# Performance work log

Measured on AMD Instinct MI355X. Metric: run time of the kernel, lower is better.

## Reference

```python
import jax, jax.numpy as jnp
import numpy as np

B, N, E, D, H, DK, DV = 1, 25000, 400000, 128, 4, 32, 32


def setup_inputs() -> dict:
    key = jax.random.key(0)
    ks = jax.random.split(key, 12)
    s = 1.0 / np.sqrt(D)
    return {
        "edge_indices": jax.random.randint(ks[0], (B, 2, E), 0, N),
        "edge_features": jax.random.normal(ks[1], (B, E, D), jnp.float32),
        "input_Q": jax.random.normal(ks[2], (B, N, D), jnp.float32),
        "input_K": jax.random.normal(ks[3], (B, N, D), jnp.float32),
        "input_V": jax.random.normal(ks[4], (B, N, D), jnp.float32),
        "W_Q": jax.random.normal(ks[5], (H * DK, D), jnp.float32) * s,
        "W_K": jax.random.normal(ks[6], (H * DK, D), jnp.float32) * s,
        "W_V": jax.random.normal(ks[7], (H * DV, D), jnp.float32) * s,
        "W_E": jax.random.normal(ks[8], (H * DV, D), jnp.float32) * s,
        "W_fc": jax.random.normal(ks[9], (D, H * DV), jnp.float32) * (1.0 / np.sqrt(H * DV)),
        "gamma": jnp.ones((D,), jnp.float32),
        "beta": jnp.zeros((D,), jnp.float32),
    }


def reference(edge_indices, edge_features, input_Q, input_K, input_V,
              W_Q, W_K, W_V, W_E, W_fc, gamma, beta):
    b, n, _ = input_Q.shape
    # projections -> [b, h, n, d]
    Q = (input_Q @ W_Q.T).reshape(b, n, H, DK).transpose(0, 2, 1, 3)
    K = (input_K @ W_K.T).reshape(b, n, H, DK).transpose(0, 2, 1, 3)
    V = (input_V @ W_V.T).reshape(b, n, H, DV).transpose(0, 2, 1, 3)
    Ef = (edge_features @ W_E.T).reshape(b, -1, H, DV).transpose(0, 2, 1, 3)  # [b,h,e,dv]
    src = edge_indices[0, 0]  # [e]
    tgt = edge_indices[0, 1]
    Qe = Q[:, :, src, :]  # [b,h,e,dk]
    Ke = K[:, :, tgt, :]
    Ve = V[:, :, tgt, :]
    scores = (Qe * Ke) / np.sqrt(DK) * Ef
    attn = jnp.exp(jnp.clip(scores.sum(-1, keepdims=True), -5.0, 5.0))  # [b,h,e,1]
    msg = attn * Ve
    out = jnp.zeros_like(Q).at[:, :, src, :].add(msg)  # scatter-add over src nodes
    coeff = jnp.zeros((b, H, n, 1), Q.dtype).at[:, :, src, :].add(attn)
    out = out / (coeff + 1e-8)
    out = out.transpose(0, 2, 1, 3).reshape(b, n, H * DV)
    out = out @ W_fc.T
    x = out + input_Q
    mu = x.mean(-1, keepdims=True)
    var = ((x - mu) ** 2).mean(-1, keepdims=True)
    y = (x - mu) / jnp.sqrt(var + 1e-5) * gamma + beta
    return y, attn
```

## Files before the change

### kernel.cpp

```cpp
#include <hip/hip_runtime.h>
#include <hip/hip_bf16.h>
#include <cstdint>
#include <cstddef>

#define EN 400000
#define NN 25000

typedef __attribute__((ext_vector_type(8))) short bf16x8;
typedef __attribute__((ext_vector_type(4))) short bf16x4;
typedef __attribute__((ext_vector_type(4))) float f32x4;
typedef __attribute__((ext_vector_type(4))) _Float16 f16x4;
typedef __attribute__((ext_vector_type(8))) _Float16 f16x8;

__device__ __forceinline__ short f2bf(float f) {
    unsigned int u = __float_as_uint(f);
    u = (u + 0x7fffu + ((u >> 16) & 1u)) >> 16;
    return (short)u;
}
__device__ __forceinline__ float bf2f(short s) {
    return __uint_as_float(((unsigned int)(unsigned short)s) << 16);
}

__device__ __forceinline__ f16x8 pin8h(f16x8 v) {
    union { f16x8 s; int i[4]; } u; u.s = v;
    const int a = (threadIdx.x & 63) << 2;
#pragma unroll
    for (int k = 0; k < 4; ++k) u.i[k] = __builtin_amdgcn_ds_bpermute(a, u.i[k]);
    return u.s;
}

__global__ __launch_bounds__(256) void convert_hist_kernel(
    const float* __restrict__ w0, const float* __restrict__ w1,
    const float* __restrict__ w2, const float* __restrict__ w3,
    const float* __restrict__ w4, _Float16* __restrict__ wf,
    short* __restrict__ wfc,
    const int* __restrict__ eidx, int* __restrict__ deg)
{
    if (blockIdx.x < 320) {
        int i = blockIdx.x * 256 + threadIdx.x;
        int w = i >> 14, off = i & 16383;
        if (w < 4) {
            const float* src = (w == 0) ? w0 : (w == 1) ? w1 : (w == 2) ? w2 : w3;
            wf[i] = (_Float16)src[off];
        } else {
            wfc[off] = f2bf(w4[off]);
        }
    } else {
        int e = (blockIdx.x - 320) * 256 + threadIdx.x;
        if (e < EN) atomicAdd(&deg[eidx[e]], 1);
    }
}

__global__ __launch_bounds__(1024) void scan_kernel(
    const int* __restrict__ deg, int* __restrict__ base)
{
    __shared__ int part[1024];
    const int t = threadIdx.x;
    const int CH = 25;
    int loc[CH];
    int s = 0;
#pragma unroll
    for (int i = 0; i < CH; ++i) {
        int idx = t * CH + i;
        loc[i] = s;
        s += (idx < NN) ? deg[idx] : 0;
    }
    part[t] = s;
    __syncthreads();
    for (int d = 1; d < 1024; d <<= 1) {
        int v = (t >= d) ? part[t - d] : 0;
        __syncthreads();
        part[t] += v;
        __syncthreads();
    }
    int off = (t > 0) ? part[t - 1] : 0;
#pragma unroll
    for (int i = 0; i < CH; ++i) {
        int idx = t * CH + i;
        if (idx < NN) base[idx] = off + loc[i];
    }
    if (t == 1023) base[NN] = part[1023];
}

__global__ __launch_bounds__(256) void scatter_kernel(
    const int* __restrict__ eidx, const int* __restrict__ base,
    int* __restrict__ cnt, int4* __restrict__ pack, int* __restrict__ tgt_csr)
{
    int e = blockIdx.x * 256 + threadIdx.x;
    if (e < EN) {
        int s = eidx[e];
        int tg = eidx[EN + e];
        int p = base[s] + atomicAdd(&cnt[s], 1);
        pack[e] = make_int4(s, tg, p, 0);
        tgt_csr[p] = tg;
    }
}

__global__ __launch_bounds__(256, 4) void proj_all_kernel(
    const float* __restrict__ inQ, const float* __restrict__ inK,
    const float* __restrict__ inV, const _Float16* __restrict__ WfBase,
    _Float16* __restrict__ Qh, _Float16* __restrict__ Kh, _Float16* __restrict__ Vh)
{
    const int mode = blockIdx.y;
    const int lane = threadIdx.x & 63;
    const int hw = threadIdx.x >> 6;
    const int el = lane & 15;
    const int g  = lane >> 4;
    const int ntiles = (NN + 15) >> 4;

    const float* X = (mode == 0) ? inQ : (mode == 1) ? inK : inV;
    const _Float16* Wf = WfBase + mode * 16384;
    _Float16* P = (mode == 0) ? Qh : (mode == 1) ? Kh : Vh;

    f16x8 wf[2][4];
#pragma unroll
    for (int dtt = 0; dtt < 2; ++dtt)
#pragma unroll
        for (int kc = 0; kc < 4; ++kc) {
            const int r = hw * 32 + ((el >> 2) * 8) + dtt * 4 + (el & 3);
            wf[dtt][kc] = pin8h(*(const f16x8*)(Wf + r * 128 + kc * 32 + g * 8));
        }

    for (int tile = blockIdx.x; tile < ntiles; tile += gridDim.x) {
        const int row = tile * 16 + el;
        const int rc = row < NN ? row : NN - 1;
        const float* xrow = X + (size_t)rc * 128;
        f32x4 acc0 = {}, acc1 = {};
#pragma unroll
        for (int kc = 0; kc < 4; ++kc) {
            const int kb = kc * 32 + g * 8;
            f32x4 x0 = *(const f32x4*)(xrow + kb);
            f32x4 x1 = *(const f32x4*)(xrow + kb + 4);
            f16x8 b;
#pragma unroll
            for (int j = 0; j < 4; ++j) { b[j] = (_Float16)x0[j]; b[4 + j] = (_Float16)x1[j]; }
            acc0 = __builtin_amdgcn_mfma_f32_16x16x32_f16(wf[0][kc], b, acc0, 0, 0, 0);
            acc1 = __builtin_amdgcn_mfma_f32_16x16x32_f16(wf[1][kc], b, acc1, 0, 0, 0);
        }
        if (row < NN) {
            f16x8 o;
#pragma unroll
            for (int j = 0; j < 4; ++j) {
                o[j]     = (_Float16)acc0[j];
                o[4 + j] = (_Float16)acc1[j];
            }
            *(f16x8*)(P + (size_t)row * 128 + hw * 32 + g * 8) = o;
        }
    }
}

__global__ __launch_bounds__(512, 2) void edge_score_kernel(
    const int4* __restrict__ pack, const float* __restrict__ efeat,
    const _Float16* __restrict__ Qh, const _Float16* __restrict__ Kh,
    const _Float16* __restrict__ WEf,
    float* __restrict__ attn_out, float* __restrict__ attn_csr)
{
    __shared__ _Float16 lds_e[2][32][136];

    const int t    = threadIdx.x;
    const int lane = t & 63;
    const int w    = t >> 6;
    const int hw   = w & 3;
    const int sub  = w >> 2;
    const int el   = lane & 15;
    const int g    = lane >> 4;
    const int se   = t >> 4;
    const int sd   = (t & 15) * 8;
    const int NT   = EN / 32;

    f16x8 wf[2][4];
#pragma unroll
    for (int dtt = 0; dtt < 2; ++dtt)
#pragma unroll
        for (int kc = 0; kc < 4; ++kc) {
            const int r = hw * 32 + ((el >> 2) * 8) + dtt * 4 + (el & 3);
            wf[dtt][kc] = pin8h(*(const f16x8*)(WEf + r * 128 + kc * 32 + g * 8));
        }

    const int dbase = hw * 32 + g * 8;
    int tile = blockIdx.x;
    int4 pk = pack[(size_t)tile * 32 + sub * 16 + el];

    {
        const float* p = efeat + ((size_t)tile * 32 + se) * 128 + sd;
        f32x4 a = *(const f32x4*)p;
        f32x4 b = *(const f32x4*)(p + 4);
        f16x8 h8;
#pragma unroll
        for (int j = 0; j < 4; ++j) {
            h8[j] = (_Float16)a[j];
            h8[4 + j] = (_Float16)b[j];
        }
        *(f16x8*)&lds_e[0][se][sd] = h8;
    }
    f32x4 eA, eB;
    int4 pk1;
    {
        const int t1 = tile + (int)gridDim.x;
        const int tl1 = (t1 < NT) ? t1 : tile;
        const float* np = efeat + ((size_t)tl1 * 32 + se) * 128 + sd;
        eA = *(const f32x4*)np;
        eB = *(const f32x4*)(np + 4);
        pk1 = pack[(size_t)tl1 * 32 + sub * 16 + el];
    }

    int buf = 0;
    while (true) {
        f16x8 q16 = *(const f16x8*)(Qh + (size_t)pk.x * 128 + dbase);
        f16x8 k16 = *(const f16x8*)(Kh + (size_t)pk.y * 128 + dbase);

        const int next = tile + (int)gridDim.x;
        const bool has_next = next < NT;
        const int n2 = next + (int)gridDim.x;
        const int tl2 = (n2 < NT) ? n2 : tile;
        const float* np2 = efeat + ((size_t)tl2 * 32 + se) * 128 + sd;
        f32x4 eAn = *(const f32x4*)np2;
        f32x4 eBn = *(const f32x4*)(np2 + 4);
        int4 pk2 = pack[(size_t)tl2 * 32 + sub * 16 + el];

        asm volatile("s_waitcnt lgkmcnt(0)" ::: "memory");
        __builtin_amdgcn_s_barrier();
        __builtin_amdgcn_sched_barrier(0);

        __builtin_amdgcn_s_setprio(1);
        f32x4 acc0 = {}, acc1 = {};
#pragma unroll
        for (int kc = 0; kc < 4; ++kc) {
            const int kb = kc * 32 + g * 8;
            f16x8 be = *(const f16x8*)&lds_e[buf][sub * 16 + el][kb];
            acc0 = __builtin_amdgcn_mfma_f32_16x16x32_f16(wf[0][kc], be, acc0, 0, 0, 0);
            acc1 = __builtin_amdgcn_mfma_f32_16x16x32_f16(wf[1][kc], be, acc1, 0, 0, 0);
        }
        __builtin_amdgcn_s_setprio(0);

        float part = 0.f;
#pragma unroll
        for (int j = 0; j < 4; ++j) {
            part += (float)q16[j]     * (float)k16[j]     * acc0[j];
            part += (float)q16[4 + j] * (float)k16[4 + j] * acc1[j];
        }
        part += __shfl_xor(part, 16, 64);
        part += __shfl_xor(part, 32, 64);
        float sc = part * 0.17677669529663687f;
        sc = fminf(5.0f, fmaxf(-5.0f, sc));
        const float a = __expf(sc);

        const int edge = tile * 32 + sub * 16 + el;
        if (g == 0) {
            attn_out[(size_t)hw * EN + edge] = a;
            attn_csr[(size_t)pk.z * 4 + hw] = a;
        }

        if (!has_next) break;

        {
            f16x8 h8;
#pragma unroll
            for (int j = 0; j < 4; ++j) {
                h8[j] = (_Float16)eA[j];
                h8[4 + j] = (_Float16)eB[j];
            }
            *(f16x8*)&lds_e[buf ^ 1][se][sd] = h8;
        }

        tile = next;
        pk = pk1;  pk1 = pk2;
        eA = eAn;  eB = eBn;
        buf ^= 1;
    }
}

__global__ __launch_bounds__(512) void node_kernel(
    const int* __restrict__ base, const int* __restrict__ tgt_csr,
    const float* __restrict__ attn_csr, const _Float16* __restrict__ Vh,
    const short* __restrict__ Wfcb, const float* __restrict__ inQ,
    const float* __restrict__ gamma, const float* __restrict__ beta,
    float* __restrict__ y)
{
    __shared__ short wlds[128 * 136];
    __shared__ float alds[32 * 132];

    const int t = threadIdx.x;
    {
        const int r = t >> 2, colb = (t & 3) * 32;
#pragma unroll
        for (int c = 0; c < 4; ++c) {
            bf16x8 w = *(const bf16x8*)(Wfcb + r * 128 + colb + c * 8);
            *(bf16x8*)(&wlds[r * 136 + colb + c * 8]) = w;
        }
    }

    const int n_l = t >> 4;
    const int el  = t & 15;
    const int node = blockIdx.x * 32 + n_l;

    int b0 = 0, b1 = 0;
    if (node < NN) { b0 = base[node]; b1 = base[node + 1]; }
    float acc[8] = {};
    float csum = 0.f;
    const int h = el >> 2;

    int p = b0;
    for (; p + 8 <= b1; p += 8) {
        int   tg[8];
        float aa[8];
        f16x8 vv[8];
#pragma unroll
        for (int u = 0; u < 8; ++u) tg[u] = tgt_csr[p + u];
#pragma unroll
        for (int u = 0; u < 8; ++u) aa[u] = attn_csr[(size_t)(p + u) * 4 + h];
#pragma unroll
        for (int u = 0; u < 8; ++u) vv[u] = *(const f16x8*)(Vh + (size_t)tg[u] * 128 + el * 8);
#pragma unroll
        for (int u = 0; u < 8; ++u) {
            csum += aa[u];
#pragma unroll
            for (int j = 0; j < 8; ++j) acc[j] += aa[u] * (float)vv[u][j];
        }
    }
    for (; p < b1; ++p) {
        const int tg = tgt_csr[p];
        const float a = attn_csr[(size_t)p * 4 + h];
        f16x8 v = *(const f16x8*)(Vh + (size_t)tg * 128 + el * 8);
        csum += a;
#pragma unroll
        for (int j = 0; j < 8; ++j) acc[j] += a * (float)v[j];
    }

    const float invc = 1.0f / (csum + 1e-8f);
#pragma unroll
    for (int j = 0; j < 8; ++j) alds[n_l * 132 + el * 8 + j] = acc[j] * invc;
    __syncthreads();

    float fc[8] = {};
#pragma unroll 4
    for (int k0 = 0; k0 < 128; k0 += 8) {
        float a8[8];
#pragma unroll
        for (int j = 0; j < 8; ++j) a8[j] = alds[n_l * 132 + k0 + j];
#pragma unroll
        for (int i = 0; i < 8; ++i) {
            const int d = el + 16 * i;
            bf16x8 w = *(const bf16x8*)(&wlds[d * 136 + k0]);
#pragma unroll
            for (int j = 0; j < 8; ++j) fc[i] += a8[j] * bf2f(w[j]);
        }
    }

    if (node < NN) {
        float x[8];
        float s = 0.f, s2 = 0.f;
#pragma unroll
        for (int i = 0; i < 8; ++i) {
            const int d = el + 16 * i;
            x[i] = fc[i] + inQ[(size_t)node * 128 + d];
            s += x[i]; s2 += x[i] * x[i];
        }
        s  += __shfl_xor(s, 1, 64);  s2 += __shfl_xor(s2, 1, 64);
        s  += __shfl_xor(s, 2, 64);  s2 += __shfl_xor(s2, 2, 64);
        s  += __shfl_xor(s, 4, 64);  s2 += __shfl_xor(s2, 4, 64);
        s  += __shfl_xor(s, 8, 64);  s2 += __shfl_xor(s2, 8, 64);
        const float mu = s * (1.0f / 128.0f);
        const float var = s2 * (1.0f / 128.0f) - mu * mu;
        const float rstd = rsqrtf(var + 1e-5f);
#pragma unroll
        for (int i = 0; i < 8; ++i) {
            const int d = el + 16 * i;
            y[(size_t)node * 128 + d] = (x[i] - mu) * rstd * gamma[d] + beta[d];
        }
    }
}

extern "C" void kernel_launch(void* const* d_in, const int* in_sizes, int n_in,
                              void* d_out, int out_size, void* d_ws, size_t ws_size,
                              hipStream_t stream) {
    const int*   eidx  = (const int*)d_in[0];
    const float* efeat = (const float*)d_in[1];
    const float* inQ   = (const float*)d_in[2];
    const float* inK   = (const float*)d_in[3];
    const float* inV   = (const float*)d_in[4];
    const float* WQ    = (const float*)d_in[5];
    const float* WK    = (const float*)d_in[6];
    const float* WV    = (const float*)d_in[7];
    const float* WE    = (const float*)d_in[8];
    const float* Wfc   = (const float*)d_in[9];
    const float* gamma = (const float*)d_in[10];
    const float* beta  = (const float*)d_in[11];

    float* y = (float*)d_out;
    float* attn_out = y + (size_t)NN * 128;

    char* ws = (char*)d_ws;
    _Float16* Qh   = (_Float16*)ws;
    _Float16* Kh   = (_Float16*)(ws + 6400000);
    _Float16* Vh   = (_Float16*)(ws + 12800000);
    _Float16* Wf   = (_Float16*)(ws + 19200000);
    short* Wfcb    = (short*)(ws + 19331072);
    float* attn_csr= (float*)(ws + 19363840);
    int*   tgt_csr = (int*)  (ws + 25763840);
    int4*  pack    = (int4*) (ws + 27363840);
    int*   deg     = (int*)  (ws + 33763840);
    int*   cnt     = (int*)  (ws + 33864192);
    int*   base    = (int*)  (ws + 33964544);

    hipMemsetAsync(deg, 0, 200704, stream);

    convert_hist_kernel<<<320 + (EN + 255) / 256, 256, 0, stream>>>(
        WQ, WK, WV, WE, Wfc, Wf, Wfcb, eidx, deg);
    scan_kernel<<<1, 1024, 0, stream>>>(deg, base);
    scatter_kernel<<<(EN + 255) / 256, 256, 0, stream>>>(eidx, base, cnt, pack, tgt_csr);

    dim3 pg(391, 3);
    proj_all_kernel<<<pg, 256, 0, stream>>>(inQ, inK, inV, Wf, Qh, Kh, Vh);

    edge_score_kernel<<<768, 512, 0, stream>>>(pack, efeat, Qh, Kh, Wf + 3 * 16384,
                                               attn_out, attn_csr);

    node_kernel<<<(NN + 31) / 32, 512, 0, stream>>>(base, tgt_csr, attn_csr, Vh,
                                                    Wfcb, inQ, gamma, beta, y);
}
```

Baseline: 218.9 us.

## Split prefix scan across blocks and degree-sort nodes for node kernel

Replaces the single-block degree scan with a three-kernel multi-block scan. It also builds a degree histogram and uses it to counting-sort node ids by degree. The node kernel then processes nodes in degree order, so the 16-lane groups in a block have similar edge-loop lengths and less load imbalance. This adds two extra kernel launches and an indirection through nodeord. The sorted order also changes which rows sit near each other in memory accesses.

```diff
diff --git a/kernel.cpp b/kernel.cpp
--- a/kernel.cpp
+++ b/kernel.cpp
@@ -7,9 +7,7 @@
 #define NN 25000
 
 typedef __attribute__((ext_vector_type(8))) short bf16x8;
-typedef __attribute__((ext_vector_type(4))) short bf16x4;
 typedef __attribute__((ext_vector_type(4))) float f32x4;
-typedef __attribute__((ext_vector_type(4))) _Float16 f16x4;
 typedef __attribute__((ext_vector_type(8))) _Float16 f16x8;
 
 __device__ __forceinline__ short f2bf(float f) {
@@ -51,35 +49,60 @@
     }
 }
 
-__global__ __launch_bounds__(1024) void scan_kernel(
-    const int* __restrict__ deg, int* __restrict__ base)
-{
-    __shared__ int part[1024];
-    const int t = threadIdx.x;
-    const int CH = 25;
-    int loc[CH];
-    int s = 0;
-#pragma unroll
-    for (int i = 0; i < CH; ++i) {
-        int idx = t * CH + i;
-        loc[i] = s;
-        s += (idx < NN) ? deg[idx] : 0;
-    }
-    part[t] = s;
+__global__ __launch_bounds__(256) void scan_a_kernel(
+    const int* __restrict__ deg, int* __restrict__ base,
+    int* __restrict__ bsum, int* __restrict__ dhist)
+{
+    __shared__ int part[256];
+    const int b = blockIdx.x, t = threadIdx.x;
+    const int idx = b * 256 + t;
+    const int d = deg[idx];
+    if (idx < NN) atomicAdd(&dhist[d < 63 ? d : 63], 1);
+    part[t] = d;
     __syncthreads();
-    for (int d = 1; d < 1024; d <<= 1) {
-        int v = (t >= d) ? part[t - d] : 0;
+    for (int o = 1; o < 256; o <<= 1) {
+        int v = (t >= o) ? part[t - o] : 0;
         __syncthreads();
         part[t] += v;
         __syncthreads();
     }
-    int off = (t > 0) ? part[t - 1] : 0;
-#pragma unroll
-    for (int i = 0; i < CH; ++i) {
-        int idx = t * CH + i;
-        if (idx < NN) base[idx] = off + loc[i];
-    }
-    if (t == 1023) base[NN] = part[1023];
+    base[idx] = part[t] - d;
+    if (t == 255) bsum[b] = part[255];
+}
+
+__global__ __launch_bounds__(128) void scan_b_kernel(
+    const int* __restrict__ bsum, int* __restrict__ boff,
+    const int* __restrict__ dhist, int* __restrict__ dbase2)
+{
+    __shared__ int s1[128], s2[128];
+    const int t = threadIdx.x;
+    const int v1 = (t < 98) ? bsum[t] : 0;
+    const int v2 = (t < 64) ? dhist[t] : 0;
+    s1[t] = v1; s2[t] = v2;
+    __syncthreads();
+    for (int o = 1; o < 128; o <<= 1) {
+        int a = (t >= o) ? s1[t - o] : 0;
+        int b = (t >= o) ? s2[t - o] : 0;
+        __syncthreads();
+        s1[t] += a; s2[t] += b;
+        __syncthreads();
+    }
+    if (t < 98) boff[t] = s1[t] - v1;
+    if (t < 64) dbase2[t] = s2[t] - v2;
+}
+
+__global__ __launch_bounds__(256) void scan_c_kernel(
+    const int* __restrict__ deg, int* __restrict__ base,
+    const int* __restrict__ boff, const int* __restrict__ dbase2,
+    int* __restrict__ dcnt, int* __restrict__ nodeord)
+{
+    const int idx = blockIdx.x * 256 + threadIdx.x;
+    base[idx] += boff[idx >> 8];
+    if (idx < NN) {
+        const int d = deg[idx] < 63 ? deg[idx] : 63;
+        const int r = dbase2[d] + atomicAdd(&dcnt[d], 1);
+        nodeord[r] = idx;
+    }
 }
 
 __global__ __launch_bounds__(256) void scatter_kernel(
@@ -271,6 +294,7 @@
 }
 
 __global__ __launch_bounds__(512) void node_kernel(
+    const int* __restrict__ nodeord,
     const int* __restrict__ base, const int* __restrict__ tgt_csr,
     const float* __restrict__ attn_csr, const _Float16* __restrict__ Vh,
     const short* __restrict__ Wfcb, const float* __restrict__ inQ,
@@ -292,7 +316,8 @@
 
     const int n_l = t >> 4;
     const int el  = t & 15;
-    const int node = blockIdx.x * 32 + n_l;
+    const int ni = blockIdx.x * 32 + n_l;
+    const int node = (ni < NN) ? nodeord[ni] : NN;
 
     int b0 = 0, b1 = 0;
     if (node < NN) { b0 = base[node]; b1 = base[node + 1]; }
@@ -401,13 +426,21 @@
     int4*  pack    = (int4*) (ws + 27363840);
     int*   deg     = (int*)  (ws + 33763840);
     int*   cnt     = (int*)  (ws + 33864192);
-    int*   base    = (int*)  (ws + 33964544);
-
-    hipMemsetAsync(deg, 0, 200704, stream);
+    int*   dhist   = (int*)  (ws + 33964544);
+    int*   dcnt    = (int*)  (ws + 33964800);
+    int*   base    = (int*)  (ws + 33965056);
+    int*   bsum    = (int*)  (ws + 34065408);
+    int*   boff    = (int*)  (ws + 34065920);
+    int*   dbase2  = (int*)  (ws + 34066432);
+    int*   nodeord = (int*)  (ws + 34066688);
+
+    hipMemsetAsync(deg, 0, 201216, stream);
 
     convert_hist_kernel<<<320 + (EN + 255) / 256, 256, 0, stream>>>(
         WQ, WK, WV, WE, Wfc, Wf, Wfcb, eidx, deg);
-    scan_kernel<<<1, 1024, 0, stream>>>(deg, base);
+    scan_a_kernel<<<98, 256, 0, stream>>>(deg, base, bsum, dhist);
+    scan_b_kernel<<<1, 128, 0, stream>>>(bsum, boff, dhist, dbase2);
+    scan_c_kernel<<<98, 256, 0, stream>>>(deg, base, boff, dbase2, dcnt, nodeord);
     scatter_kernel<<<(EN + 255) / 256, 256, 0, stream>>>(eidx, base, cnt, pack, tgt_csr);
 
     dim3 pg(391, 3);
@@ -416,6 +449,6 @@
     edge_score_kernel<<<768, 512, 0, stream>>>(pack, efeat, Qh, Kh, Wf + 3 * 16384,
                                                attn_out, attn_csr);
 
-    node_kernel<<<(NN + 31) / 32, 512, 0, stream>>>(base, tgt_csr, attn_csr, Vh,
+    node_kernel<<<(NN + 31) / 32, 512, 0, stream>>>(nodeord, base, tgt_csr, attn_csr, Vh,
                                                     Wfcb, inQ, gamma, beta, y);
 }
```

After: 338.8 us. 54.7% more time.
